# Performance work log

Hardware: AMD Instinct MI355X
Metric: run time of the kernel (lower is better)

The kernel has to match this reference:

```python
import jax, jax.numpy as jnp
import numpy as np

BS = 4096
FD = 768   # feature_dim
PD = 500   # proj_dim
ZD = 300   # z_dim
R = 10     # retrieval_num
U = 10     # retrieval_user_num
N_PER = 3 + 2 * R + U  # 33 nodes per sample


def _lin(x, w, b):
    return x @ w.T + b


def _build_incidence(bs, r, u):
    # Faithful to get_hyper_edge_index_and_weight: 4 group edges per sample
    # plus R pair edges that (as in the original code) omit the batch bias,
    # i.e. always reference sample-0 nodes. dhg.Hypergraph dedups duplicate
    # edges, so the R pair edges appear once.
    n = 3 + 2 * r + u
    node_list, edge_list = [], []
    e = 0
    for b in range(bs):
        o = b * n
        groups = [
            list(range(o, o + 3)),
            list(range(o + 3, o + 3 + r)) + [o],
            list(range(o + 3 + r, o + 3 + 2 * r)) + [o + 1],
            list(range(o + 3 + 2 * r, o + n)) + [o + 2],
        ]
        for g in groups:
            node_list.extend(g)
            edge_list.extend([e] * len(g))
            e += 1
    for i in range(r):
        node_list.extend([3 + i, 3 + r + i])
        edge_list.extend([e, e])
        e += 1
    return np.asarray(node_list, np.int32), np.asarray(edge_list, np.int32), e


def setup_inputs() -> dict:
    key = jax.random.key(0)
    ks = jax.random.split(key, 32)

    def rn(k, shape, s=1.0):
        return jax.random.normal(k, shape, dtype=jnp.float32) * s

    inp = {
        "visual_feature": rn(ks[0], (BS, 1, FD)),
        "textual_feature": rn(ks[1], (BS, 1, FD)),
        "similarity": rn(ks[2], (BS, R)),
        "retrieved_visual_feature": rn(ks[3], (BS, R, 1, FD)),
        "retrieved_textual_feature": rn(ks[4], (BS, R, FD)),
        "retrieved_label": jax.random.uniform(ks[5], (BS, R, 1), dtype=jnp.float32),
        "user": rn(ks[6], (BS, FD)),
        "retrieved_user": rn(ks[7], (BS, U, FD)),
        "retrieved_user_similarity": rn(ks[8], (BS, U)),
        # learned params (0.02-scaled normal init)
        "vis_w": rn(ks[9], (PD, FD), 0.02), "vis_b": jnp.zeros((PD,), jnp.float32),
        "txt_w": rn(ks[10], (PD, FD), 0.02), "txt_b": jnp.zeros((PD,), jnp.float32),
        "usr_w": rn(ks[11], (PD, FD), 0.02), "usr_b": jnp.zeros((PD,), jnp.float32),
        "rvis_w": rn(ks[12], (PD, FD), 0.02), "rvis_b": jnp.zeros((PD,), jnp.float32),
        "rtxt_w": rn(ks[13], (PD, FD), 0.02), "rtxt_b": jnp.zeros((PD,), jnp.float32),
        "rusr_w": rn(ks[14], (PD, FD), 0.02), "rusr_b": jnp.zeros((PD,), jnp.float32),
        "hg_w": rn(ks[15], (ZD, PD), 0.02), "hg_b": jnp.zeros((ZD,), jnp.float32),
        "lbl_w": rn(ks[16], (ZD, 1), 0.02), "lbl_b": jnp.zeros((ZD,), jnp.float32),
        "p1_w": rn(ks[17], (800, ZD * 7), 0.02), "p1_b": jnp.zeros((800,), jnp.float32),
        "p2_w": rn(ks[18], (200, 800), 0.02), "p2_b": jnp.zeros((200,), jnp.float32),
        "p3_w": rn(ks[19], (1, 200), 0.02), "p3_b": jnp.zeros((1,), jnp.float32),
    }
    return inp


def reference(visual_feature, textual_feature, similarity, retrieved_visual_feature,
              retrieved_textual_feature, retrieved_label, user, retrieved_user,
              retrieved_user_similarity,
              vis_w, vis_b, txt_w, txt_b, usr_w, usr_b,
              rvis_w, rvis_b, rtxt_w, rtxt_b, rusr_w, rusr_b,
              hg_w, hg_b, lbl_w, lbl_b,
              p1_w, p1_b, p2_w, p2_b, p3_w, p3_b):
    bs = visual_feature.shape[0]
    # dense tanh embeddings -> per-sample node feature block [bs, 33, 500]
    t = jnp.tanh(_lin(textual_feature, txt_w, txt_b))
    v = jnp.tanh(_lin(visual_feature, vis_w, vis_b))
    u = jnp.tanh(_lin(user[:, None, :], usr_w, usr_b))
    rt = jnp.tanh(_lin(retrieved_textual_feature, rtxt_w, rtxt_b))
    rv = jnp.tanh(_lin(retrieved_visual_feature[:, :, 0, :], rvis_w, rvis_b))
    ru = jnp.tanh(_lin(retrieved_user, rusr_w, rusr_b))
    X = jnp.concatenate([t, v, u, rt, rv, ru], axis=1).reshape(-1, PD)  # [bs*33, 500]

    # hypergraph conv (HGNN+ layer, softmax_then_sum over unit incidence == mean)
    node_ids, edge_ids, E = _build_incidence(bs, R, U)  # static, built at trace time
    N = X.shape[0]
    Xt = _lin(X, hg_w, hg_b)  # theta: [N, 300]
    ones = jnp.ones(node_ids.shape[0], jnp.float32)
    deg_e = jax.ops.segment_sum(ones, edge_ids, num_segments=E)
    Y = jax.ops.segment_sum(Xt[node_ids], edge_ids, num_segments=E) / deg_e[:, None]
    deg_v = jax.ops.segment_sum(ones, node_ids, num_segments=N)
    Xo = jax.ops.segment_sum(Y[edge_ids], node_ids, num_segments=N) / deg_v[:, None]
    Xo = jax.nn.relu(Xo).reshape(bs, N_PER, ZD)

    # retrieval aggregation: softmax-weighted sums over retrieved sets
    sim = jax.nn.softmax(similarity, axis=1)                      # [bs, R]
    usim = jax.nn.softmax(retrieved_user_similarity, axis=1)      # [bs, U]
    rt_agg = jnp.einsum('br,brd->bd', sim, Xo[:, 3:3 + R, :])
    rv_agg = jnp.einsum('br,brd->bd', sim, Xo[:, 3 + R:3 + 2 * R, :])
    ru_agg = jnp.einsum('br,brd->bd', usim, Xo[:, 3 + 2 * R:3 + 2 * R + U, :])
    lbl_agg = jnp.einsum('br,bro->bo', sim, retrieved_label)      # [bs, 1]
    lbl_emb = jax.nn.relu(_lin(lbl_agg, lbl_w, lbl_b))            # [bs, 300]

    feat = jnp.concatenate(
        [Xo[:, 0, :], Xo[:, 1, :], Xo[:, 2, :], rv_agg, rt_agg, ru_agg, lbl_emb], axis=1)
    h = jax.nn.relu(_lin(feat, p1_w, p1_b))
    h = jax.nn.relu(_lin(h, p2_w, p2_b))
    out = jax.nn.sigmoid(_lin(h, p3_w, p3_b))  # [bs, 1]
    return out
```

## Files before the change

### kernel.cpp

```cpp
#include <hip/hip_runtime.h>
#include <math.h>

#define BS 4096
#define FD 768
#define PD 500
#define ZD 300
#define RNUM 10

typedef short bf16x8 __attribute__((ext_vector_type(8)));
typedef float f32x4 __attribute__((ext_vector_type(4)));

__device__ __forceinline__ unsigned int fbits(float f) {
  union { float f; unsigned int u; } v; v.f = f; return v.u;
}

__device__ __forceinline__ unsigned int pack2bf(float f0, float f1) {
  unsigned int u0 = fbits(f0) + 0x8000u;
  unsigned int u1 = fbits(f1) + 0x8000u;
  return __builtin_amdgcn_perm(u1, u0, 0x07060302u);
}

#define BM 128
#define BN 64
#define BK 16
#define TM 8
#define TN 4
template <int ACT>
__global__ __launch_bounds__(256) void gemm_kernel(
    const float* __restrict__ A, const float* __restrict__ W,
    const float* __restrict__ bias, float* __restrict__ C,
    int M, int N, int K) {
  __shared__ float As[BK][BM + 4];
  __shared__ float Bs[BK][BN + 4];
  const int m0 = blockIdx.x * BM;
  const int n0 = blockIdx.y * BN;
  const int tid = threadIdx.x;
  const int tx = tid & 15;
  const int ty = tid >> 4;
  float acc[TM][TN];
#pragma unroll
  for (int i = 0; i < TM; i++)
#pragma unroll
    for (int j = 0; j < TN; j++) acc[i][j] = 0.f;
  const int l_row = tid >> 2;
  const int l_k4 = (tid & 3) * 4;
  for (int k0 = 0; k0 < K; k0 += BK) {
#pragma unroll
    for (int half = 0; half < 2; ++half) {
      int m = m0 + l_row + half * 64;
      int k = k0 + l_k4;
      float4 v = make_float4(0.f, 0.f, 0.f, 0.f);
      if (m < M && k + 4 <= K) v = *(const float4*)(A + (size_t)m * K + k);
      As[l_k4 + 0][l_row + half * 64] = v.x;
      As[l_k4 + 1][l_row + half * 64] = v.y;
      As[l_k4 + 2][l_row + half * 64] = v.z;
      As[l_k4 + 3][l_row + half * 64] = v.w;
    }
    {
      int n = n0 + l_row;
      int k = k0 + l_k4;
      float4 v = make_float4(0.f, 0.f, 0.f, 0.f);
      if (n < N && k + 4 <= K) v = *(const float4*)(W + (size_t)n * K + k);
      Bs[l_k4 + 0][l_row] = v.x;
      Bs[l_k4 + 1][l_row] = v.y;
      Bs[l_k4 + 2][l_row] = v.z;
      Bs[l_k4 + 3][l_row] = v.w;
    }
    __syncthreads();
#pragma unroll
    for (int k = 0; k < BK; k++) {
      float a[TM], b[TN];
#pragma unroll
      for (int i = 0; i < TM; i++) a[i] = As[k][ty * TM + i];
#pragma unroll
      for (int j = 0; j < TN; j++) b[j] = Bs[k][tx * TN + j];
#pragma unroll
      for (int i = 0; i < TM; i++)
#pragma unroll
        for (int j = 0; j < TN; j++) acc[i][j] += a[i] * b[j];
    }
    __syncthreads();
  }
#pragma unroll
  for (int i = 0; i < TM; i++) {
    int m = m0 + ty * TM + i;
    if (m >= M) continue;
#pragma unroll
    for (int j = 0; j < TN; j++) {
      int n = n0 + tx * TN + j;
      if (n >= N) continue;
      float v = acc[i][j] + bias[n];
      if (ACT == 1) v = fmaxf(v, 0.f);
      C[(size_t)m * N + n] = v;
    }
  }
}

__global__ __launch_bounds__(256) void padcast(
    const float* __restrict__ src, unsigned short* __restrict__ dst,
    int rs, int cs, int rd, int cd) {
  int i = blockIdx.x * 256 + threadIdx.x;
  if (i >= rd * cd) return;
  int r = i / cd, c = i - r * cd;
  float v = (r < rs && c < cs) ? src[(size_t)r * cs + c] : 0.f;
  dst[i] = (unsigned short)((fbits(v) + 0x8000u) >> 16);
}

template <int ACT>
__global__ __launch_bounds__(256) void mfma_gemm(
    const float* __restrict__ A, int lda, int Ka,
    const unsigned short* __restrict__ B, int Kp,
    const float* __restrict__ bias, float* __restrict__ C, int Nout) {
  __shared__ unsigned short ldsA[2][128 * 32];
  __shared__ unsigned short ldsB[2][128 * 32];
  const int tid = threadIdx.x;
  const int n0 = blockIdx.x * 128;
  const int m0 = blockIdx.y * 128;

  const int arow = tid >> 1;
  const int ahalf = (tid & 1) << 4;
  const int ag = (tid & 1) << 1;
  const int aswz = (arow >> 1) & 3;
  const int aw0 = (arow * 4 + ((ag | 0) ^ aswz)) * 8;
  const int aw1 = (arow * 4 + ((ag | 1) ^ aswz)) * 8;
  const float* aptr = A + (size_t)(m0 + arow) * lda;
  const unsigned short* bptr = B + (size_t)(n0 + arow) * Kp + ahalf;

  const int lane = tid & 63;
  const int wave = tid >> 6;
  const int wm = (wave >> 1) << 6;
  const int wn = (wave & 1) << 6;
  const int r16 = lane & 15;
  const int kq = lane >> 4;

  int afoff[4], bfoff[4];
#pragma unroll
  for (int i = 0; i < 4; i++) {
    int rowA = wm + i * 16 + r16;
    afoff[i] = (rowA * 4 + (kq ^ ((rowA >> 1) & 3))) * 8;
    int rowB = wn + i * 16 + r16;
    bfoff[i] = (rowB * 4 + (kq ^ ((rowB >> 1) & 3))) * 8;
  }

  f32x4 acc[4][4] = {};
  const int NT = Kp >> 5;

  float4 f[4];
  uint4 bv0, bv1;
#pragma unroll
  for (int q = 0; q < 4; q++) {
    int k = ahalf + q * 4;
    f[q] = (k < Ka) ? *(const float4*)(aptr + k) : make_float4(0.f, 0.f, 0.f, 0.f);
  }
  bv0 = *(const uint4*)(bptr + 0);
  bv1 = *(const uint4*)(bptr + 8);
  {
    uint4 w0, w1;
    w0.x = pack2bf(f[0].x, f[0].y); w0.y = pack2bf(f[0].z, f[0].w);
    w0.z = pack2bf(f[1].x, f[1].y); w0.w = pack2bf(f[1].z, f[1].w);
    w1.x = pack2bf(f[2].x, f[2].y); w1.y = pack2bf(f[2].z, f[2].w);
    w1.z = pack2bf(f[3].x, f[3].y); w1.w = pack2bf(f[3].z, f[3].w);
    *(uint4*)&ldsA[0][aw0] = w0;
    *(uint4*)&ldsA[0][aw1] = w1;
    *(uint4*)&ldsB[0][aw0] = bv0;
    *(uint4*)&ldsB[0][aw1] = bv1;
  }

#pragma unroll 2
  for (int t = 0; t < NT; ++t) {
    const int cb = t & 1;
    asm volatile("s_waitcnt lgkmcnt(0)" ::: "memory");
    __builtin_amdgcn_s_barrier();
    if (t + 1 < NT) {
      const int k0 = (t + 1) << 5;
#pragma unroll
      for (int q = 0; q < 4; q++) {
        int k = k0 + ahalf + q * 4;
        f[q] = (k < Ka) ? *(const float4*)(aptr + k)
                        : make_float4(0.f, 0.f, 0.f, 0.f);
      }
      bv0 = *(const uint4*)(bptr + k0);
      bv1 = *(const uint4*)(bptr + k0 + 8);
    }
    bf16x8 a[4], b[4];
#pragma unroll
    for (int i = 0; i < 4; i++) a[i] = *(const bf16x8*)&ldsA[cb][afoff[i]];
#pragma unroll
    for (int i = 0; i < 4; i++) b[i] = *(const bf16x8*)&ldsB[cb][bfoff[i]];
#pragma unroll
    for (int i = 0; i < 4; i++)
#pragma unroll
      for (int j = 0; j < 4; j++)
        acc[i][j] = __builtin_amdgcn_mfma_f32_16x16x32_bf16(a[i], b[j], acc[i][j], 0, 0, 0);
    if (t + 1 < NT) {
      uint4 w0, w1;
      w0.x = pack2bf(f[0].x, f[0].y); w0.y = pack2bf(f[0].z, f[0].w);
      w0.z = pack2bf(f[1].x, f[1].y); w0.w = pack2bf(f[1].z, f[1].w);
      w1.x = pack2bf(f[2].x, f[2].y); w1.y = pack2bf(f[2].z, f[2].w);
      w1.z = pack2bf(f[3].x, f[3].y); w1.w = pack2bf(f[3].z, f[3].w);
      *(uint4*)&ldsA[cb ^ 1][aw0] = w0;
      *(uint4*)&ldsA[cb ^ 1][aw1] = w1;
      *(uint4*)&ldsB[cb ^ 1][aw0] = bv0;
      *(uint4*)&ldsB[cb ^ 1][aw1] = bv1;
    }
  }

#pragma unroll
  for (int j = 0; j < 4; j++) {
    int n = n0 + wn + j * 16 + r16;
    if (n >= Nout) continue;
    float bi = bias[n];
#pragma unroll
    for (int i = 0; i < 4; i++) {
#pragma unroll
      for (int r = 0; r < 4; r++) {
        int m = m0 + wm + i * 16 + kq * 4 + r;
        float v = acc[i][j][r] + bi;
        if (ACT == 1) v = fmaxf(v, 0.f);
        C[(size_t)m * Nout + n] = v;
      }
    }
  }
}

struct EmbedArgs {
  const float* A[6];
  const float* bias[6];
};

__global__ __launch_bounds__(512, 2) void embed_mfma(
    EmbedArgs ea, const unsigned short* __restrict__ Wbf,
    float* __restrict__ S, float* __restrict__ E0) {
  __shared__ unsigned short ldsA[2][128 * 32];
  __shared__ unsigned short ldsB[2][512 * 32];
  const int tid = threadIdx.x;
  const int m0 = blockIdx.x * 128;

  int g, base;
  if (m0 < 4096) { g = 0; base = 0; }
  else if (m0 < 8192) { g = 1; base = 4096; }
  else if (m0 < 12288) { g = 2; base = 8192; }
  else if (m0 < 53248) { g = 3; base = 12288; }
  else if (m0 < 94208) { g = 4; base = 53248; }
  else { g = 5; base = 94208; }

  const int arow = tid >> 2;
  const int aq = tid & 3;
  const int aswz = (arow >> 1) & 3;
  const int awoff = (arow * 4 + (aq ^ aswz)) * 8;
  const float* aptr = ea.A[g] + (size_t)(m0 - base + arow) * FD + aq * 8;

  const int brow = tid;
  const int bswz = (brow >> 1) & 3;
  int bwoff[4];
#pragma unroll
  for (int q = 0; q < 4; q++) bwoff[q] = (brow * 4 + (q ^ bswz)) * 8;
  const unsigned short* bptr = Wbf + (size_t)g * 512 * FD + (size_t)brow * FD;

  const int lane = tid & 63;
  const int wave = tid >> 6;
  const int wm = (wave >> 2) << 6;
  const int wn = (wave & 3) << 7;
  const int r16 = lane & 15;
  const int kq = lane >> 4;

  int afoff[4], bfoff[8];
#pragma unroll
  for (int i = 0; i < 4; i++) {
    int rowA = wm + i * 16 + r16;
    afoff[i] = (rowA * 4 + (kq ^ ((rowA >> 1) & 3))) * 8;
  }
#pragma unroll
  for (int j = 0; j < 8; j++) {
    int rowB = wn + j * 16 + r16;
    bfoff[j] = (rowB * 4 + (kq ^ ((rowB >> 1) & 3))) * 8;
  }

  f32x4 acc[4][8] = {};

  float4 fa0 = *(const float4*)(aptr + 0);
  float4 fa1 = *(const float4*)(aptr + 4);
  uint4 bv[4];
#pragma unroll
  for (int q = 0; q < 4; q++) bv[q] = *(const uint4*)(bptr + q * 8);
  {
    uint4 aw;
    aw.x = pack2bf(fa0.x, fa0.y); aw.y = pack2bf(fa0.z, fa0.w);
    aw.z = pack2bf(fa1.x, fa1.y); aw.w = pack2bf(fa1.z, fa1.w);
    *(uint4*)&ldsA[0][awoff] = aw;
#pragma unroll
    for (int q = 0; q < 4; q++) *(uint4*)&ldsB[0][bwoff[q]] = bv[q];
  }

  const int NT = FD / 32;
#pragma unroll 2
  for (int t = 0; t < NT; ++t) {
    const int cb = t & 1;
    asm volatile("s_waitcnt lgkmcnt(0)" ::: "memory");
    __builtin_amdgcn_s_barrier();
    if (t + 1 < NT) {
      const float* ap = aptr + (t + 1) * 32;
      fa0 = *(const float4*)(ap + 0);
      fa1 = *(const float4*)(ap + 4);
      const unsigned short* bp = bptr + (t + 1) * 32;
#pragma unroll
      for (int q = 0; q < 4; q++) bv[q] = *(const uint4*)(bp + q * 8);
    }
    bf16x8 a[4], b[8];
#pragma unroll
    for (int i = 0; i < 4; i++) a[i] = *(const bf16x8*)&ldsA[cb][afoff[i]];
#pragma unroll
    for (int j = 0; j < 8; j++) b[j] = *(const bf16x8*)&ldsB[cb][bfoff[j]];
#pragma unroll
    for (int i = 0; i < 4; i++)
#pragma unroll
      for (int j = 0; j < 8; j++)
        acc[i][j] = __builtin_amdgcn_mfma_f32_16x16x32_bf16(a[i], b[j], acc[i][j], 0, 0, 0);
    if (t + 1 < NT) {
      uint4 aw;
      aw.x = pack2bf(fa0.x, fa0.y); aw.y = pack2bf(fa0.z, fa0.w);
      aw.z = pack2bf(fa1.x, fa1.y); aw.w = pack2bf(fa1.z, fa1.w);
      *(uint4*)&ldsA[cb ^ 1][awoff] = aw;
#pragma unroll
      for (int q = 0; q < 4; q++) *(uint4*)&ldsB[cb ^ 1][bwoff[q]] = bv[q];
    }
  }

  const float* bias = ea.bias[g];
  if (g < 3) {
#pragma unroll
    for (int j = 0; j < 8; j++) {
      int n = wn + j * 16 + r16;
      if (n >= PD) continue;
      float bi = bias[n];
#pragma unroll
      for (int i = 0; i < 4; i++) {
#pragma unroll
        for (int r = 0; r < 4; r++) {
          int rl = m0 - base + wm + i * 16 + kq * 4 + r;
          S[((size_t)g * BS + rl) * PD + n] = tanhf(acc[i][j][r] + bi);
        }
      }
    }
    return;
  }

  const int R0 = m0 - base;
  const int b0 = R0 / 10;
  const int b1 = (R0 + 127) / 10;
  const int ng = b1 - b0 + 1;
  float* red = (float*)&ldsB[0][0];
  const int myc = wave & 3;
  __syncthreads();
#pragma unroll
  for (int ch = 0; ch < 8; ++ch) {
    if ((ch >> 1) == myc) {
#pragma unroll
      for (int jj = 0; jj < 4; jj++) {
        int j = ((ch & 1) << 2) + jj;
        int n = wn + j * 16 + r16;
        int cl = (jj << 4) + r16;
        float bi = (n < PD) ? bias[n] : 0.f;
#pragma unroll
        for (int i = 0; i < 4; i++) {
#pragma unroll
          for (int r = 0; r < 4; r++) {
            int row = wm + i * 16 + kq * 4 + r;
            red[row * 68 + cl] = acc[i][j][r] + bi;
          }
        }
      }
    }
    __syncthreads();
    for (int task = tid; task < ng * 64; task += 512) {
      int cl = task & 63;
      int bb = b0 + (task >> 6);
      int n = (ch << 6) + cl;
      if (n < PD) {
        int rlo = bb * 10 - R0;
        int rhi = rlo + 9;
        int lo = rlo < 0 ? 0 : rlo;
        int hi = rhi > 127 ? 127 : rhi;
        float s = 0.f;
        for (int r = lo; r <= hi; r++) s += tanhf(red[r * 68 + cl]);
        size_t idx = ((size_t)g * BS + bb) * PD + n;
        if (hi - lo == 9) S[idx] = s;
        else atomicAdd(&S[idx], s);
        if (g != 5 && bb == 0 && R0 == 0) {
#pragma unroll
          for (int rr = 0; rr < 10; rr++)
            E0[((size_t)(g - 3) * 10 + rr) * PD + n] = tanhf(red[rr * 68 + cl]);
        }
      }
    }
    __syncthreads();
  }
}

__global__ __launch_bounds__(256) void means_kernel(
    const float* __restrict__ S, float* __restrict__ Mn) {
  const int total = 4 * BS * PD;
  for (int i = blockIdx.x * blockDim.x + threadIdx.x; i < total;
       i += gridDim.x * blockDim.x) {
    int m = i / PD;
    int k = i - m * PD;
    int b = m >> 2, e = m & 3;
    float v;
    const size_t o = (size_t)b * PD + k;
    if (e == 0)
      v = (S[o] + S[(size_t)BS * PD + o] + S[2 * (size_t)BS * PD + o]) * (1.f / 3.f);
    else if (e == 1)
      v = (S[3 * (size_t)BS * PD + o] + S[o]) * (1.f / 11.f);
    else if (e == 2)
      v = (S[4 * (size_t)BS * PD + o] + S[(size_t)BS * PD + o]) * (1.f / 11.f);
    else
      v = (S[5 * (size_t)BS * PD + o] + S[2 * (size_t)BS * PD + o]) * (1.f / 11.f);
    Mn[i] = v;
  }
}

__global__ __launch_bounds__(256) void xte_kernel(
    const float* __restrict__ E0, const float* __restrict__ hg_w,
    const float* __restrict__ hg_b, float* __restrict__ XtE) {
  const int i = blockIdx.x;
  __shared__ float row[PD];
  for (int k = threadIdx.x; k < PD; k += 256) row[k] = E0[(size_t)i * PD + k];
  __syncthreads();
  for (int n = threadIdx.x; n < ZD; n += 256) {
    float s = 0.f;
    const float* w = hg_w + (size_t)n * PD;
    for (int k = 0; k < PD; k++) s += row[k] * w[k];
    XtE[(size_t)i * ZD + n] = s + hg_b[n];
  }
}

__global__ __launch_bounds__(256) void feat_kernel(
    const float* __restrict__ Y, const float* __restrict__ XtE,
    const float* __restrict__ sim_in, const float* __restrict__ label,
    const float* __restrict__ lbl_w, const float* __restrict__ lbl_b,
    float* __restrict__ feat) {
  const int b = blockIdx.x;
  __shared__ float w[RNUM];
  __shared__ float lbl_agg_s;
  if (threadIdx.x == 0) {
    float s[RNUM], mx = -1e30f;
    for (int r = 0; r < RNUM; r++) {
      s[r] = sim_in[(size_t)b * RNUM + r];
      mx = fmaxf(mx, s[r]);
    }
    float sum = 0.f;
    for (int r = 0; r < RNUM; r++) { s[r] = expf(s[r] - mx); sum += s[r]; }
    float la = 0.f;
    for (int r = 0; r < RNUM; r++) {
      w[r] = s[r] / sum;
      la += w[r] * label[(size_t)b * RNUM + r];
    }
    lbl_agg_s = la;
  }
  __syncthreads();
  const float* Yb = Y + (size_t)b * 4 * ZD;
  float* fb = feat + (size_t)b * 7 * ZD;
  const float la = lbl_agg_s;
  for (int n = threadIdx.x; n < ZD; n += blockDim.x) {
    float y0 = Yb[n], y1 = Yb[ZD + n], y2 = Yb[2 * ZD + n], y3 = Yb[3 * ZD + n];
    fb[n] = fmaxf(0.5f * (y0 + y1), 0.f);
    fb[ZD + n] = fmaxf(0.5f * (y0 + y2), 0.f);
    fb[2 * ZD + n] = fmaxf(0.5f * (y0 + y3), 0.f);
    float rv, rt;
    if (b == 0) {
      rv = 0.f; rt = 0.f;
      for (int r = 0; r < RNUM; r++) {
        float yp = 0.5f * (XtE[(size_t)r * ZD + n] + XtE[(size_t)(10 + r) * ZD + n]);
        rt += w[r] * fmaxf(0.5f * (y1 + yp), 0.f);
        rv += w[r] * fmaxf(0.5f * (y2 + yp), 0.f);
      }
    } else {
      rt = fmaxf(y1, 0.f);
      rv = fmaxf(y2, 0.f);
    }
    fb[3 * ZD + n] = rv;
    fb[4 * ZD + n] = rt;
    fb[5 * ZD + n] = fmaxf(y3, 0.f);
    fb[6 * ZD + n] = fmaxf(la * lbl_w[n] + lbl_b[n], 0.f);
  }
}

__global__ __launch_bounds__(256) void head_kernel(
    const float* __restrict__ h2, const float* __restrict__ p3_w,
    const float* __restrict__ p3_b, float* __restrict__ out) {
  const int wave = (blockIdx.x * blockDim.x + threadIdx.x) >> 6;
  const int lane = threadIdx.x & 63;
  if (wave >= BS) return;
  const float* row = h2 + (size_t)wave * 200;
  float s = 0.f;
  for (int k = lane; k < 200; k += 64) s += row[k] * p3_w[k];
#pragma unroll
  for (int off = 32; off; off >>= 1) s += __shfl_down(s, off, 64);
  if (lane == 0) out[wave] = 1.f / (1.f + expf(-(s + p3_b[0])));
}

extern "C" void kernel_launch(void* const* d_in, const int* in_sizes, int n_in,
                              void* d_out, int out_size, void* d_ws,
                              size_t ws_size, hipStream_t stream) {
  (void)in_sizes; (void)n_in; (void)out_size; (void)ws_size;

  const float* visual = (const float*)d_in[0];
  const float* textual = (const float*)d_in[1];
  const float* similarity = (const float*)d_in[2];
  const float* r_visual = (const float*)d_in[3];
  const float* r_textual = (const float*)d_in[4];
  const float* r_label = (const float*)d_in[5];
  const float* user = (const float*)d_in[6];
  const float* r_user = (const float*)d_in[7];
  const float* vis_w = (const float*)d_in[9];
  const float* vis_b = (const float*)d_in[10];
  const float* txt_w = (const float*)d_in[11];
  const float* txt_b = (const float*)d_in[12];
  const float* usr_w = (const float*)d_in[13];
  const float* usr_b = (const float*)d_in[14];
  const float* rvis_w = (const float*)d_in[15];
  const float* rvis_b = (const float*)d_in[16];
  const float* rtxt_w = (const float*)d_in[17];
  const float* rtxt_b = (const float*)d_in[18];
  const float* rusr_w = (const float*)d_in[19];
  const float* rusr_b = (const float*)d_in[20];
  const float* hg_w = (const float*)d_in[21];
  const float* hg_b = (const float*)d_in[22];
  const float* lbl_w = (const float*)d_in[23];
  const float* lbl_b = (const float*)d_in[24];
  const float* p1_w = (const float*)d_in[25];
  const float* p1_b = (const float*)d_in[26];
  const float* p2_w = (const float*)d_in[27];
  const float* p2_b = (const float*)d_in[28];
  const float* p3_w = (const float*)d_in[29];
  const float* p3_b = (const float*)d_in[30];
  float* out = (float*)d_out;

  float* ws = (float*)d_ws;
  float* S = ws;
  float* E0 = S + (size_t)6 * BS * PD;
  float* XtE = E0 + 20 * PD;
  float* Mn = XtE + 20 * ZD;
  float* Y = Mn + (size_t)4 * BS * PD;
  float* feat = Y + (size_t)4 * BS * ZD;
  float* h1 = feat + (size_t)BS * 7 * ZD;
  float* h2 = h1 + (size_t)BS * 800;
  unsigned short* Wbf = (unsigned short*)(h2 + (size_t)BS * 200);
  unsigned short* hgwbf = Wbf + (size_t)6 * 512 * FD;
  unsigned short* p1wbf = hgwbf + (size_t)384 * 512;

  const float* ew[6] = {txt_w, vis_w, usr_w, rtxt_w, rvis_w, rusr_w};
  for (int g = 0; g < 6; g++) {
    padcast<<<(512 * FD + 255) / 256, 256, 0, stream>>>(
        ew[g], Wbf + (size_t)g * 512 * FD, PD, FD, 512, FD);
  }
  padcast<<<(384 * 512 + 255) / 256, 256, 0, stream>>>(hg_w, hgwbf, ZD, PD, 384, 512);
  padcast<<<(896 * 2112 + 255) / 256, 256, 0, stream>>>(p1_w, p1wbf, 800, 2100, 896, 2112);

  hipMemsetAsync(S + (size_t)3 * BS * PD, 0, (size_t)3 * BS * PD * sizeof(float),
                 stream);

  EmbedArgs ea;
  ea.A[0] = textual;  ea.bias[0] = txt_b;
  ea.A[1] = visual;   ea.bias[1] = vis_b;
  ea.A[2] = user;     ea.bias[2] = usr_b;
  ea.A[3] = r_textual; ea.bias[3] = rtxt_b;
  ea.A[4] = r_visual;  ea.bias[4] = rvis_b;
  ea.A[5] = r_user;    ea.bias[5] = rusr_b;

  embed_mfma<<<dim3(135168 / 128), 512, 0, stream>>>(ea, Wbf, S, E0);
  xte_kernel<<<20, 256, 0, stream>>>(E0, hg_w, hg_b, XtE);
  means_kernel<<<4096, 256, 0, stream>>>(S, Mn);
  mfma_gemm<0><<<dim3(3, 16384 / 128), 256, 0, stream>>>(
      Mn, PD, PD, hgwbf, 512, hg_b, Y, ZD);
  feat_kernel<<<BS, 256, 0, stream>>>(Y, XtE, similarity, r_label, lbl_w, lbl_b,
                                      feat);
  mfma_gemm<1><<<dim3(7, BS / 128), 256, 0, stream>>>(
      feat, 2100, 2100, p1wbf, 2112, p1_b, h1, 800);
  gemm_kernel<1><<<dim3(BS / BM, (200 + BN - 1) / BN), 256, 0, stream>>>(
      h1, p2_w, p2_b, h2, BS, 200, 800);
  head_kernel<<<BS * 64 / 256, 256, 0, stream>>>(h2, p3_w, p3_b, out);
}
```

Before: 1.170 ms.

## Pre-tile bf16 weights into swizzled LDS order for contiguous B loads

Weight cast kernels now write bf16 weights already arranged per K-tile and per 128/512-row block in the swizzled LDS layout, so the GEMM kernels load B with fully contiguous per-thread 16-byte reads and store them straight into LDS without swizzle math. The intermediate S buffer row stride is padded from 500 to 512. The aim is better coalescing of the weight reads and simpler addressing. It also changes the workspace layout and the offsets of the cast kernels, and the cast kernel now reads 8 floats with a strided gather.

```diff
diff --git a/kernel.cpp b/kernel.cpp
--- a/kernel.cpp
+++ b/kernel.cpp
@@ -6,6 +6,7 @@
 #define PD 500
 #define ZD 300
 #define RNUM 10
+#define SD 512
 
 typedef short bf16x8 __attribute__((ext_vector_type(8)));
 typedef float f32x4 __attribute__((ext_vector_type(4)));
@@ -96,20 +97,39 @@
   }
 }
 
-__global__ __launch_bounds__(256) void padcast(
+__global__ __launch_bounds__(256) void padcast_tileB(
     const float* __restrict__ src, unsigned short* __restrict__ dst,
-    int rs, int cs, int rd, int cd) {
+    int rs, int cs, int rowsPerTile, int nRowTiles, int NT) {
+  const int total = nRowTiles * NT * rowsPerTile * 4;
   int i = blockIdx.x * 256 + threadIdx.x;
-  if (i >= rd * cd) return;
-  int r = i / cd, c = i - r * cd;
-  float v = (r < rs && c < cs) ? src[(size_t)r * cs + c] : 0.f;
-  dst[i] = (unsigned short)((fbits(v) + 0x8000u) >> 16);
+  if (i >= total) return;
+  const int gpt = rowsPerTile * 4;
+  int nb = i / (NT * gpt);
+  int rem1 = i - nb * NT * gpt;
+  int t = rem1 / gpt;
+  int rem = rem1 - t * gpt;
+  int row = rem >> 2;
+  int slot = rem & 3;
+  int gq = slot ^ ((row >> 1) & 3);
+  int grow = nb * rowsPerTile + row;
+  float f[8];
+#pragma unroll
+  for (int e = 0; e < 8; e++) {
+    int k = t * 32 + gq * 8 + e;
+    f[e] = (grow < rs && k < cs) ? src[(size_t)grow * cs + k] : 0.f;
+  }
+  uint4 o;
+  o.x = pack2bf(f[0], f[1]);
+  o.y = pack2bf(f[2], f[3]);
+  o.z = pack2bf(f[4], f[5]);
+  o.w = pack2bf(f[6], f[7]);
+  *(uint4*)(dst + (size_t)i * 8) = o;
 }
 
 template <int ACT>
 __global__ __launch_bounds__(256) void mfma_gemm(
     const float* __restrict__ A, int lda, int Ka,
-    const unsigned short* __restrict__ B, int Kp,
+    const unsigned short* __restrict__ B, int NT,
     const float* __restrict__ bias, float* __restrict__ C, int Nout) {
   __shared__ unsigned short ldsA[2][128 * 32];
   __shared__ unsigned short ldsB[2][128 * 32];
@@ -124,7 +144,7 @@
   const int aw0 = (arow * 4 + ((ag | 0) ^ aswz)) * 8;
   const int aw1 = (arow * 4 + ((ag | 1) ^ aswz)) * 8;
   const float* aptr = A + (size_t)(m0 + arow) * lda;
-  const unsigned short* bptr = B + (size_t)(n0 + arow) * Kp + ahalf;
+  const unsigned short* bbase = B + (size_t)blockIdx.x * NT * 4096 + (size_t)tid * 8;
 
   const int lane = tid & 63;
   const int wave = tid >> 6;
@@ -143,7 +163,6 @@
   }
 
   f32x4 acc[4][4] = {};
-  const int NT = Kp >> 5;
 
   float4 f[4];
   uint4 bv0, bv1;
@@ -152,8 +171,8 @@
     int k = ahalf + q * 4;
     f[q] = (k < Ka) ? *(const float4*)(aptr + k) : make_float4(0.f, 0.f, 0.f, 0.f);
   }
-  bv0 = *(const uint4*)(bptr + 0);
-  bv1 = *(const uint4*)(bptr + 8);
+  bv0 = *(const uint4*)(bbase + 0);
+  bv1 = *(const uint4*)(bbase + 2048);
   {
     uint4 w0, w1;
     w0.x = pack2bf(f[0].x, f[0].y); w0.y = pack2bf(f[0].z, f[0].w);
@@ -162,8 +181,8 @@
     w1.z = pack2bf(f[3].x, f[3].y); w1.w = pack2bf(f[3].z, f[3].w);
     *(uint4*)&ldsA[0][aw0] = w0;
     *(uint4*)&ldsA[0][aw1] = w1;
-    *(uint4*)&ldsB[0][aw0] = bv0;
-    *(uint4*)&ldsB[0][aw1] = bv1;
+    *(uint4*)&ldsB[0][tid * 8] = bv0;
+    *(uint4*)&ldsB[0][tid * 8 + 2048] = bv1;
   }
 
 #pragma unroll 2
@@ -179,8 +198,8 @@
         f[q] = (k < Ka) ? *(const float4*)(aptr + k)
                         : make_float4(0.f, 0.f, 0.f, 0.f);
       }
-      bv0 = *(const uint4*)(bptr + k0);
-      bv1 = *(const uint4*)(bptr + k0 + 8);
+      bv0 = *(const uint4*)(bbase + (size_t)(t + 1) * 4096);
+      bv1 = *(const uint4*)(bbase + (size_t)(t + 1) * 4096 + 2048);
     }
     bf16x8 a[4], b[4];
 #pragma unroll
@@ -200,8 +219,8 @@
       w1.z = pack2bf(f[3].x, f[3].y); w1.w = pack2bf(f[3].z, f[3].w);
       *(uint4*)&ldsA[cb ^ 1][aw0] = w0;
       *(uint4*)&ldsA[cb ^ 1][aw1] = w1;
-      *(uint4*)&ldsB[cb ^ 1][aw0] = bv0;
-      *(uint4*)&ldsB[cb ^ 1][aw1] = bv1;
+      *(uint4*)&ldsB[cb ^ 1][tid * 8] = bv0;
+      *(uint4*)&ldsB[cb ^ 1][tid * 8 + 2048] = bv1;
     }
   }
 
@@ -250,12 +269,7 @@
   const int awoff = (arow * 4 + (aq ^ aswz)) * 8;
   const float* aptr = ea.A[g] + (size_t)(m0 - base + arow) * FD + aq * 8;
 
-  const int brow = tid;
-  const int bswz = (brow >> 1) & 3;
-  int bwoff[4];
-#pragma unroll
-  for (int q = 0; q < 4; q++) bwoff[q] = (brow * 4 + (q ^ bswz)) * 8;
-  const unsigned short* bptr = Wbf + (size_t)g * 512 * FD + (size_t)brow * FD;
+  const unsigned short* bbase = Wbf + (size_t)g * (24 * 16384) + (size_t)tid * 8;
 
   const int lane = tid & 63;
   const int wave = tid >> 6;
@@ -282,14 +296,14 @@
   float4 fa1 = *(const float4*)(aptr + 4);
   uint4 bv[4];
 #pragma unroll
-  for (int q = 0; q < 4; q++) bv[q] = *(const uint4*)(bptr + q * 8);
+  for (int q = 0; q < 4; q++) bv[q] = *(const uint4*)(bbase + q * 4096);
   {
     uint4 aw;
     aw.x = pack2bf(fa0.x, fa0.y); aw.y = pack2bf(fa0.z, fa0.w);
     aw.z = pack2bf(fa1.x, fa1.y); aw.w = pack2bf(fa1.z, fa1.w);
     *(uint4*)&ldsA[0][awoff] = aw;
 #pragma unroll
-    for (int q = 0; q < 4; q++) *(uint4*)&ldsB[0][bwoff[q]] = bv[q];
+    for (int q = 0; q < 4; q++) *(uint4*)&ldsB[0][tid * 8 + q * 4096] = bv[q];
   }
 
   const int NT = FD / 32;
@@ -302,9 +316,9 @@
       const float* ap = aptr + (t + 1) * 32;
       fa0 = *(const float4*)(ap + 0);
       fa1 = *(const float4*)(ap + 4);
-      const unsigned short* bp = bptr + (t + 1) * 32;
-#pragma unroll
-      for (int q = 0; q < 4; q++) bv[q] = *(const uint4*)(bp + q * 8);
+      const unsigned short* bp = bbase + (size_t)(t + 1) * 16384;
+#pragma unroll
+      for (int q = 0; q < 4; q++) bv[q] = *(const uint4*)(bp + q * 4096);
     }
     bf16x8 a[4], b[8];
 #pragma unroll
@@ -322,7 +336,8 @@
       aw.z = pack2bf(fa1.x, fa1.y); aw.w = pack2bf(fa1.z, fa1.w);
       *(uint4*)&ldsA[cb ^ 1][awoff] = aw;
 #pragma unroll
-      for (int q = 0; q < 4; q++) *(uint4*)&ldsB[cb ^ 1][bwoff[q]] = bv[q];
+      for (int q = 0; q < 4; q++)
+        *(uint4*)&ldsB[cb ^ 1][tid * 8 + q * 4096] = bv[q];
     }
   }
 
@@ -338,7 +353,7 @@
 #pragma unroll
         for (int r = 0; r < 4; r++) {
           int rl = m0 - base + wm + i * 16 + kq * 4 + r;
-          S[((size_t)g * BS + rl) * PD + n] = tanhf(acc[i][j][r] + bi);
+          S[((size_t)g * BS + rl) * SD + n] = tanhf(acc[i][j][r] + bi);
         }
       }
     }
@@ -383,7 +398,7 @@
         int hi = rhi > 127 ? 127 : rhi;
         float s = 0.f;
         for (int r = lo; r <= hi; r++) s += tanhf(red[r * 68 + cl]);
-        size_t idx = ((size_t)g * BS + bb) * PD + n;
+        size_t idx = ((size_t)g * BS + bb) * SD + n;
         if (hi - lo == 9) S[idx] = s;
         else atomicAdd(&S[idx], s);
         if (g != 5 && bb == 0 && R0 == 0) {
@@ -400,21 +415,22 @@
 __global__ __launch_bounds__(256) void means_kernel(
     const float* __restrict__ S, float* __restrict__ Mn) {
   const int total = 4 * BS * PD;
+  const size_t P = (size_t)BS * SD;
   for (int i = blockIdx.x * blockDim.x + threadIdx.x; i < total;
        i += gridDim.x * blockDim.x) {
     int m = i / PD;
     int k = i - m * PD;
     int b = m >> 2, e = m & 3;
     float v;
-    const size_t o = (size_t)b * PD + k;
+    const size_t o = (size_t)b * SD + k;
     if (e == 0)
-      v = (S[o] + S[(size_t)BS * PD + o] + S[2 * (size_t)BS * PD + o]) * (1.f / 3.f);
+      v = (S[o] + S[P + o] + S[2 * P + o]) * (1.f / 3.f);
     else if (e == 1)
-      v = (S[3 * (size_t)BS * PD + o] + S[o]) * (1.f / 11.f);
+      v = (S[3 * P + o] + S[o]) * (1.f / 11.f);
     else if (e == 2)
-      v = (S[4 * (size_t)BS * PD + o] + S[(size_t)BS * PD + o]) * (1.f / 11.f);
+      v = (S[4 * P + o] + S[P + o]) * (1.f / 11.f);
     else
-      v = (S[5 * (size_t)BS * PD + o] + S[2 * (size_t)BS * PD + o]) * (1.f / 11.f);
+      v = (S[5 * P + o] + S[2 * P + o]) * (1.f / 11.f);
     Mn[i] = v;
   }
 }
@@ -538,7 +554,7 @@
 
   float* ws = (float*)d_ws;
   float* S = ws;
-  float* E0 = S + (size_t)6 * BS * PD;
+  float* E0 = S + (size_t)6 * BS * SD;
   float* XtE = E0 + 20 * PD;
   float* Mn = XtE + 20 * ZD;
   float* Y = Mn + (size_t)4 * BS * PD;
@@ -546,18 +562,20 @@
   float* h1 = feat + (size_t)BS * 7 * ZD;
   float* h2 = h1 + (size_t)BS * 800;
   unsigned short* Wbf = (unsigned short*)(h2 + (size_t)BS * 200);
-  unsigned short* hgwbf = Wbf + (size_t)6 * 512 * FD;
-  unsigned short* p1wbf = hgwbf + (size_t)384 * 512;
+  unsigned short* hgwbf = Wbf + (size_t)6 * 24 * 16384;
+  unsigned short* p1wbf = hgwbf + (size_t)3 * 16 * 4096;
 
   const float* ew[6] = {txt_w, vis_w, usr_w, rtxt_w, rvis_w, rusr_w};
   for (int g = 0; g < 6; g++) {
-    padcast<<<(512 * FD + 255) / 256, 256, 0, stream>>>(
-        ew[g], Wbf + (size_t)g * 512 * FD, PD, FD, 512, FD);
-  }
-  padcast<<<(384 * 512 + 255) / 256, 256, 0, stream>>>(hg_w, hgwbf, ZD, PD, 384, 512);
-  padcast<<<(896 * 2112 + 255) / 256, 256, 0, stream>>>(p1_w, p1wbf, 800, 2100, 896, 2112);
-
-  hipMemsetAsync(S + (size_t)3 * BS * PD, 0, (size_t)3 * BS * PD * sizeof(float),
+    padcast_tileB<<<(24 * 512 * 4 + 255) / 256, 256, 0, stream>>>(
+        ew[g], Wbf + (size_t)g * 24 * 16384, PD, FD, 512, 1, 24);
+  }
+  padcast_tileB<<<(3 * 16 * 128 * 4 + 255) / 256, 256, 0, stream>>>(
+      hg_w, hgwbf, ZD, PD, 128, 3, 16);
+  padcast_tileB<<<(7 * 66 * 128 * 4 + 255) / 256, 256, 0, stream>>>(
+      p1_w, p1wbf, 800, 2100, 128, 7, 66);
+
+  hipMemsetAsync(S + (size_t)3 * BS * SD, 0, (size_t)3 * BS * SD * sizeof(float),
                  stream);
 
   EmbedArgs ea;
@@ -572,11 +590,11 @@
   xte_kernel<<<20, 256, 0, stream>>>(E0, hg_w, hg_b, XtE);
   means_kernel<<<4096, 256, 0, stream>>>(S, Mn);
   mfma_gemm<0><<<dim3(3, 16384 / 128), 256, 0, stream>>>(
-      Mn, PD, PD, hgwbf, 512, hg_b, Y, ZD);
+      Mn, PD, PD, hgwbf, 16, hg_b, Y, ZD);
   feat_kernel<<<BS, 256, 0, stream>>>(Y, XtE, similarity, r_label, lbl_w, lbl_b,
                                       feat);
   mfma_gemm<1><<<dim3(7, BS / 128), 256, 0, stream>>>(
-      feat, 2100, 2100, p1wbf, 2112, p1_b, h1, 800);
+      feat, 2100, 2100, p1wbf, 66, p1_b, h1, 800);
   gemm_kernel<1><<<dim3(BS / BM, (200 + BN - 1) / BN), 256, 0, stream>>>(
       h1, p2_w, p2_b, h2, BS, 200, 800);
   head_kernel<<<BS * 64 / 256, 256, 0, stream>>>(h2, p3_w, p3_b, out);
```

Measured after the change: 1.075 ms. -8.2%, faster.
